# Kernel tuning notes

Measured on AMD Instinct MI355X. Metric: run time of the kernel, lower is better.

The kernel has to match this reference:

```python
import jax, jax.numpy as jnp
import numpy as np

B, L, D = 2, 2048, 1024
H = 16
HD = D // H  # 64


def _orthogonal_projection(key, d, m):
    g = jax.random.normal(key, (d, m), dtype=jnp.float32)
    q, r = jnp.linalg.qr(g)
    s = jnp.sign(jnp.diagonal(r))
    s = jnp.where(s == 0, 1.0, s)
    q = q * s[None, :]
    # preserve_variance=True
    return q * np.sqrt(d / m)


def setup_inputs() -> dict:
    key = jax.random.key(0)
    ks = jax.random.split(key, 8)
    x = jax.random.normal(ks[0], (B, L, D), dtype=jnp.float32)
    p = jax.random.normal(ks[1], (B, L, D), dtype=jnp.float32)
    s = 1.0 / np.sqrt(D)
    W_qkv = jax.random.uniform(ks[2], (3 * D, D), dtype=jnp.float32, minval=-s, maxval=s)
    b_qkv = jax.random.uniform(ks[3], (3 * D,), dtype=jnp.float32, minval=-s, maxval=s)
    W_out = jax.random.uniform(ks[4], (D, D), dtype=jnp.float32, minval=-s, maxval=s)
    b_out = jax.random.uniform(ks[5], (D,), dtype=jnp.float32, minval=-s, maxval=s)
    proj = _orthogonal_projection(ks[6], D, D // 2)
    return {"x": x, "p": p, "W_qkv": W_qkv, "b_qkv": b_qkv,
            "W_out": W_out, "b_out": b_out, "proj": proj}


def reference(x, p, W_qkv, b_qkv, W_out, b_out, proj):
    # QKV projection: (B,L,D) -> (B,L,3,H,HD)
    qkv = (jnp.einsum('bld,ed->ble', x, W_qkv) + b_qkv).reshape(B, L, 3, H, HD)
    q, k, v = qkv[:, :, 0], qkv[:, :, 1], qkv[:, :, 2]

    # Collaborative rotary phases from conditioning tokens: (B,L,H,HD/2)
    phases = (p @ proj).reshape(B, L, H, HD // 2)  # phase_scale = 1.0
    cos, sin = jnp.cos(phases), jnp.sin(phases)

    half = HD // 2
    # non-interleaved rotary: split head_dim into two halves
    def rot(t):
        t1, t2 = t[..., :half], t[..., half:]
        return jnp.concatenate([t1 * cos - t2 * sin, t1 * sin + t2 * cos], axis=-1)

    q, k = rot(q), rot(k)

    scale = HD ** -0.5
    scores = jnp.einsum('bqhd,bkhd->bhqk', q, k) * scale
    attn = jax.nn.softmax(scores, axis=-1)
    out = jnp.einsum('bhqk,bkhd->bqhd', attn, v).reshape(B, L, D)
    return jnp.einsum('bld,ed->ble', out, W_out) + b_out
```

## Files before the change

kernel.cpp:

```cpp
#include <hip/hip_runtime.h>
#include <hip/hip_bf16.h>
#include <math.h>

namespace {
constexpr int Bb = 2;
constexpr int Ll = 2048;
constexpr int Dd = 1024;
constexpr int Hh = 16;
constexpr int NT = Bb * Ll;
constexpr int D3 = 3 * Dd;
constexpr int PH = Dd / 2;
constexpr int LDK = 72;
}

typedef __attribute__((ext_vector_type(8))) short bf16x8;
typedef __attribute__((ext_vector_type(4))) short bf16x4;
typedef __attribute__((ext_vector_type(4))) float f32x4;

#if defined(__has_builtin)
#if __has_builtin(__builtin_amdgcn_mfma_f32_16x16x16bf16_1k)
#define HAVE_MFMA16 1
#endif
#endif

__device__ inline unsigned pack2bf(float a, float b) {
  __hip_bfloat162 t = __float22bfloat162_rn(float2{a, b});
  union { __hip_bfloat162 h; unsigned u; } cv; cv.h = t;
  return cv.u;
}

__device__ inline bf16x4 u2bf4(uint2 u) {
  union { uint2 u; bf16x4 v; } c; c.u = u; return c.v;
}

__device__ inline f32x4 pv_mfma(bf16x4 va, bf16x4 vb, f32x4 c) {
#ifdef HAVE_MFMA16
  return __builtin_amdgcn_mfma_f32_16x16x16bf16_1k(va, vb, c, 0, 0, 0);
#else
  const bf16x8 a8 = {va[0], va[1], va[2], va[3], 0, 0, 0, 0};
  const bf16x8 b8 = {vb[0], vb[1], vb[2], vb[3], 0, 0, 0, 0};
  return __builtin_amdgcn_mfma_f32_16x16x32_bf16(a8, b8, c, 0, 0, 0);
#endif
}

__device__ inline void async_cp16(const void* gsrc, void* ldst) {
  __builtin_amdgcn_global_load_lds(
      (const __attribute__((address_space(1))) unsigned int*)gsrc,
      (__attribute__((address_space(3))) unsigned int*)ldst, 16, 0, 0);
}

__global__ __launch_bounds__(256) void cast4_kernel(
    const float4* __restrict__ src, uint2* __restrict__ dst, int n4)
{
  const int i = blockIdx.x * 256 + threadIdx.x;
  if (i >= n4) return;
  const float4 f = src[i];
  dst[i] = make_uint2(pack2bf(f.x, f.y), pack2bf(f.z, f.w));
}

__global__ __launch_bounds__(256) void split_cast_kernel(
    const float4* __restrict__ src, uint2* __restrict__ hi, uint2* __restrict__ lo, int n4)
{
  const int i = blockIdx.x * 256 + threadIdx.x;
  if (i >= n4) return;
  const float4 f = src[i];
  float hf[4], lf[4];
  const float ff[4] = {f.x, f.y, f.z, f.w};
#pragma unroll
  for (int j = 0; j < 4; ++j) {
    const __hip_bfloat16 h = __float2bfloat16(ff[j]);
    hf[j] = __bfloat162float(h);
    lf[j] = ff[j] - hf[j];
  }
  hi[i] = make_uint2(pack2bf(hf[0], hf[1]), pack2bf(hf[2], hf[3]));
  lo[i] = make_uint2(pack2bf(lf[0], lf[1]), pack2bf(lf[2], lf[3]));
}

__global__ __launch_bounds__(256) void trans_split_kernel(
    const float* __restrict__ proj, short* __restrict__ th, short* __restrict__ tl)
{
  __shared__ float Ls[64][65];
  const int tid = threadIdx.x;
  const int d0 = blockIdx.x * 64, m0 = blockIdx.y * 64;
  const int r = tid >> 4, c4 = (tid & 15) * 4;
#pragma unroll
  for (int it = 0; it < 4; ++it) {
    const int row = it * 16 + r;
    const float4 v = *(const float4*)&proj[(size_t)(d0 + row) * PH + m0 + c4];
    Ls[row][c4] = v.x; Ls[row][c4+1] = v.y; Ls[row][c4+2] = v.z; Ls[row][c4+3] = v.w;
  }
  __syncthreads();
#pragma unroll
  for (int it = 0; it < 4; ++it) {
    const int row = it * 16 + r;
    float hf[4], lf[4];
#pragma unroll
    for (int j = 0; j < 4; ++j) {
      const float v = Ls[c4 + j][row];
      const __hip_bfloat16 h = __float2bfloat16(v);
      hf[j] = __bfloat162float(h);
      lf[j] = v - hf[j];
    }
    *(uint2*)&th[(size_t)(m0 + row) * Dd + d0 + c4] = make_uint2(pack2bf(hf[0], hf[1]), pack2bf(hf[2], hf[3]));
    *(uint2*)&tl[(size_t)(m0 + row) * Dd + d0 + c4] = make_uint2(pack2bf(lf[0], lf[1]), pack2bf(lf[2], lf[3]));
  }
}

__global__ __launch_bounds__(256) void gemm_nn_split(
    const short* __restrict__ Ah_g, const short* __restrict__ Al_g,
    const short* __restrict__ Wh_g, const short* __restrict__ Wl_g,
    float* __restrict__ C)
{
  __shared__ __align__(16) short Ah[64 * 32], Al[64 * 32], Wh[64 * 32], Wl[64 * 32];
  const int tid = threadIdx.x;
  const int w = tid >> 6, lane = tid & 63;
  const int l15 = lane & 15, quad = lane >> 4;
  const int wn = w >> 1, wm = w & 1;
  const int n0 = blockIdx.y * 64, m0 = blockIdx.x * 64;

  const int row = tid >> 2, cc = tid & 3;
  const int ksw = (cc ^ (row & 3)) * 8;
  const short* gAh = Ah_g + (size_t)(n0 + row) * Dd + ksw;
  const short* gAl = Al_g + (size_t)(n0 + row) * Dd + ksw;
  const short* gWh = Wh_g + (size_t)(m0 + row) * Dd + ksw;
  const short* gWl = Wl_g + (size_t)(m0 + row) * Dd + ksw;
  short* lAh = Ah + tid * 8;
  short* lAl = Al + tid * 8;
  short* lWh = Wh + tid * 8;
  short* lWl = Wl + tid * 8;

  f32x4 acc[2][2];
#pragma unroll
  for (int i = 0; i < 2; ++i)
#pragma unroll
    for (int j = 0; j < 2; ++j) acc[i][j] = f32x4{0.f, 0.f, 0.f, 0.f};

  const int swq = (quad ^ (l15 & 3)) * 8;

  for (int k0 = 0; k0 < Dd; k0 += 32) {
    __syncthreads();
    async_cp16(gAh + k0, lAh);
    async_cp16(gAl + k0, lAl);
    async_cp16(gWh + k0, lWh);
    async_cp16(gWl + k0, lWl);
    __syncthreads();

    bf16x8 ah[2], al[2], wh[2], wl[2];
#pragma unroll
    for (int i = 0; i < 2; ++i) {
      ah[i] = *(const bf16x8*)&Ah[(wn * 32 + i * 16 + l15) * 32 + swq];
      al[i] = *(const bf16x8*)&Al[(wn * 32 + i * 16 + l15) * 32 + swq];
    }
#pragma unroll
    for (int j = 0; j < 2; ++j) {
      wh[j] = *(const bf16x8*)&Wh[(wm * 32 + j * 16 + l15) * 32 + swq];
      wl[j] = *(const bf16x8*)&Wl[(wm * 32 + j * 16 + l15) * 32 + swq];
    }
#pragma unroll
    for (int i = 0; i < 2; ++i)
#pragma unroll
      for (int j = 0; j < 2; ++j) {
        acc[i][j] = __builtin_amdgcn_mfma_f32_16x16x32_bf16(ah[i], wh[j], acc[i][j], 0, 0, 0);
        acc[i][j] = __builtin_amdgcn_mfma_f32_16x16x32_bf16(ah[i], wl[j], acc[i][j], 0, 0, 0);
        acc[i][j] = __builtin_amdgcn_mfma_f32_16x16x32_bf16(al[i], wh[j], acc[i][j], 0, 0, 0);
      }
  }

#pragma unroll
  for (int i = 0; i < 2; ++i)
#pragma unroll
    for (int r = 0; r < 4; ++r) {
      float* crow = C + (size_t)(n0 + wn * 32 + i * 16 + quad * 4 + r) * PH + m0 + wm * 32 + l15;
#pragma unroll
      for (int j = 0; j < 2; ++j) crow[j * 16] = acc[i][j][r];
    }
}

__global__ __launch_bounds__(256) void gemm_bt_bf16(
    const __hip_bfloat16* __restrict__ A, const __hip_bfloat16* __restrict__ W,
    const float* __restrict__ bias, float* __restrict__ C, int K, int M)
{
  __shared__ __align__(16) short As[128 * 32];
  __shared__ __align__(16) short Ws[128 * 32];
  const int tid = threadIdx.x;
  const int w = tid >> 6, lane = tid & 63;
  const int l15 = lane & 15, quad = lane >> 4;
  const int wn = w >> 1, wm = w & 1;
  const int n0 = blockIdx.y * 128, m0 = blockIdx.x * 128;

  const int row = tid >> 2, cc = tid & 3;
  const int ksw = (cc ^ (row & 3)) * 8;
  const short* gA  = (const short*)A + (size_t)(n0 + row) * K + ksw;
  const short* gW  = (const short*)W + (size_t)(m0 + row) * K + ksw;
  short* lA  = As + tid * 8;
  short* lA2 = As + 2048 + tid * 8;
  short* lW  = Ws + tid * 8;
  short* lW2 = Ws + 2048 + tid * 8;

  f32x4 acc[4][4];
#pragma unroll
  for (int i = 0; i < 4; ++i)
#pragma unroll
    for (int j = 0; j < 4; ++j) acc[i][j] = f32x4{0.f, 0.f, 0.f, 0.f};

  const int swq = (quad ^ (l15 & 3)) * 8;

  for (int k0 = 0; k0 < K; k0 += 32) {
    __syncthreads();
    async_cp16(gA + k0, lA);
    async_cp16(gA + 64 * K + k0, lA2);
    async_cp16(gW + k0, lW);
    async_cp16(gW + 64 * K + k0, lW2);
    __syncthreads();

    bf16x8 af[4], bf[4];
#pragma unroll
    for (int i = 0; i < 4; ++i)
      af[i] = *(const bf16x8*)&As[(wn * 64 + i * 16 + l15) * 32 + swq];
#pragma unroll
    for (int j = 0; j < 4; ++j)
      bf[j] = *(const bf16x8*)&Ws[(wm * 64 + j * 16 + l15) * 32 + swq];
#pragma unroll
    for (int i = 0; i < 4; ++i)
#pragma unroll
      for (int j = 0; j < 4; ++j)
        acc[i][j] = __builtin_amdgcn_mfma_f32_16x16x32_bf16(af[i], bf[j], acc[i][j], 0, 0, 0);
  }

  float bv[4];
#pragma unroll
  for (int j = 0; j < 4; ++j) bv[j] = bias[m0 + wm * 64 + j * 16 + l15];
#pragma unroll
  for (int i = 0; i < 4; ++i)
#pragma unroll
    for (int r = 0; r < 4; ++r) {
      float* crow = C + (size_t)(n0 + wn * 64 + i * 16 + quad * 4 + r) * M + m0 + wm * 64 + l15;
#pragma unroll
      for (int j = 0; j < 4; ++j) crow[j * 16] = acc[i][j][r] + bv[j];
    }
}

__global__ __launch_bounds__(256) void rot_cast_kernel(
    const float* __restrict__ phases, const float* __restrict__ qkv,
    __hip_bfloat16* __restrict__ q_bf, __hip_bfloat16* __restrict__ k_bf)
{
  const int gid = blockIdx.x * 256 + threadIdx.x;
  const int i = gid & 31;
  const int h = (gid >> 5) & 15;
  const int n = gid >> 9;
  const float ph = phases[n * PH + h * 32 + i];
  float sn, cs;
  __sincosf(ph, &sn, &cs);
  const int base = n * D3 + h * 64 + i;
  const float q1 = qkv[base], q2 = qkv[base + 32];
  const float k1 = qkv[base + Dd], k2 = qkv[base + Dd + 32];
  const float SC = 0.18033688011112042f;
  const int ob = n * Dd + h * 64 + i;
  q_bf[ob]      = __float2bfloat16((q1 * cs - q2 * sn) * SC);
  q_bf[ob + 32] = __float2bfloat16((q1 * sn + q2 * cs) * SC);
  k_bf[ob]      = __float2bfloat16(k1 * cs - k2 * sn);
  k_bf[ob + 32] = __float2bfloat16(k1 * sn + k2 * cs);
}

__global__ __launch_bounds__(256) void vtrans_kernel(
    const float* __restrict__ qkv, __hip_bfloat16* __restrict__ vt_g)
{
  __shared__ __align__(16) short Vl[64 * LDK];
  const int tid = threadIdx.x;
  const int tt = blockIdx.x;
  const int bh = blockIdx.y;
  const int b = bh >> 4, h = bh & 15;

  {
    const int tok = tid >> 2, ds = tid & 3;
    const float* src = qkv + (size_t)(b * Ll + tt * 64 + tok) * D3 + 2 * Dd + h * 64 + ds * 16;
    unsigned* dstw = (unsigned*)&Vl[tok * LDK + ds * 16];
#pragma unroll
    for (int jj = 0; jj < 4; ++jj) {
      const float4 f = *(const float4*)(src + jj * 4);
      dstw[jj*2]   = pack2bf(f.x, f.y);
      dstw[jj*2+1] = pack2bf(f.z, f.w);
    }
  }
  __syncthreads();
  {
    const int d = tid >> 2, seg = tid & 3;
    unsigned ow[8];
#pragma unroll
    for (int j = 0; j < 8; ++j) {
      const unsigned short a = (unsigned short)Vl[(seg*16 + 2*j)     * LDK + d];
      const unsigned short c = (unsigned short)Vl[(seg*16 + 2*j + 1) * LDK + d];
      ow[j] = (unsigned)a | ((unsigned)c << 16);
    }
    unsigned* dst = (unsigned*)(vt_g + ((size_t)(bh * 64 + d)) * Ll + tt * 64 + seg * 16);
    *(uint4*)(dst)     = make_uint4(ow[0], ow[1], ow[2], ow[3]);
    *(uint4*)(dst + 4) = make_uint4(ow[4], ow[5], ow[6], ow[7]);
  }
}

__global__ __launch_bounds__(256) void attn_mfma(
    const __hip_bfloat16* __restrict__ q_bf,
    const __hip_bfloat16* __restrict__ k_bf,
    const __hip_bfloat16* __restrict__ vt_g,
    __hip_bfloat16* __restrict__ aout)
{
  __shared__ __align__(16) short Ks[64 * LDK];
  __shared__ __align__(16) short Vt[64 * LDK];

  const int tid = threadIdx.x;
  const int w = tid >> 6;
  const int lane = tid & 63;
  const int l15 = lane & 15;
  const int quad = lane >> 4;

  const int q0 = blockIdx.x * 128;
  const int bh = blockIdx.y;
  const int b = bh >> 4, h = bh & 15;

  bf16x8 qfrag[2][2];
#pragma unroll
  for (int qg = 0; qg < 2; ++qg)
#pragma unroll
    for (int kh = 0; kh < 2; ++kh) {
      const size_t qrow = (size_t)(b * Ll + q0 + w * 32 + qg * 16 + l15);
      qfrag[qg][kh] = *(const bf16x8*)(q_bf + qrow * Dd + h * 64 + kh * 32 + quad * 8);
    }

  f32x4 acc[4][2];
#pragma unroll
  for (int dt = 0; dt < 4; ++dt)
#pragma unroll
    for (int qg = 0; qg < 2; ++qg) acc[dt][qg] = f32x4{0.f, 0.f, 0.f, 0.f};
  float l_acc[2] = {0.f, 0.f};

  const int srow = tid >> 2, sseg = tid & 3;
  const __hip_bfloat16* kbase = k_bf + (size_t)(b * Ll + srow) * Dd + h * 64 + sseg * 16;
  const __hip_bfloat16* vbase = vt_g + ((size_t)(bh * 64 + srow)) * Ll + sseg * 16;

  for (int kt = 0; kt < Ll / 64; ++kt) {
    __syncthreads();
    {
      const uint4* kg = (const uint4*)(kbase + (size_t)kt * 64 * Dd);
      *(uint4*)&Ks[srow * LDK + sseg * 16]     = kg[0];
      *(uint4*)&Ks[srow * LDK + sseg * 16 + 8] = kg[1];
      const uint4* vg = (const uint4*)(vbase + kt * 64);
      *(uint4*)&Vt[srow * LDK + sseg * 16]     = vg[0];
      *(uint4*)&Vt[srow * LDK + sseg * 16 + 8] = vg[1];
    }
    __syncthreads();

    f32x4 s[4][2];
#pragma unroll
    for (int n = 0; n < 4; ++n)
#pragma unroll
      for (int qg = 0; qg < 2; ++qg) s[n][qg] = f32x4{0.f, 0.f, 0.f, 0.f};
#pragma unroll
    for (int n = 0; n < 4; ++n)
#pragma unroll
      for (int kh = 0; kh < 2; ++kh) {
        const bf16x8 af = *(const bf16x8*)&Ks[(n * 16 + l15) * LDK + kh * 32 + quad * 8];
        s[n][0] = __builtin_amdgcn_mfma_f32_16x16x32_bf16(af, qfrag[0][kh], s[n][0], 0, 0, 0);
        s[n][1] = __builtin_amdgcn_mfma_f32_16x16x32_bf16(af, qfrag[1][kh], s[n][1], 0, 0, 0);
      }

    uint2 bq[4][2];
#pragma unroll
    for (int qg = 0; qg < 2; ++qg)
#pragma unroll
      for (int n = 0; n < 4; ++n) {
        const float p0 = __builtin_amdgcn_exp2f(s[n][qg][0]);
        const float p1 = __builtin_amdgcn_exp2f(s[n][qg][1]);
        const float p2 = __builtin_amdgcn_exp2f(s[n][qg][2]);
        const float p3 = __builtin_amdgcn_exp2f(s[n][qg][3]);
        l_acc[qg] += (p0 + p1) + (p2 + p3);
        bq[n][qg] = make_uint2(pack2bf(p0, p1), pack2bf(p2, p3));
      }

#pragma unroll
    for (int n = 0; n < 4; ++n) {
      const bf16x4 pb0 = u2bf4(bq[n][0]);
      const bf16x4 pb1 = u2bf4(bq[n][1]);
#pragma unroll
      for (int dt = 0; dt < 4; ++dt) {
        const bf16x4 va = *(const bf16x4*)&Vt[(dt * 16 + l15) * LDK + n * 16 + quad * 4];
        acc[dt][0] = pv_mfma(va, pb0, acc[dt][0]);
        acc[dt][1] = pv_mfma(va, pb1, acc[dt][1]);
      }
    }
  }

#pragma unroll
  for (int qg = 0; qg < 2; ++qg) {
    float l = l_acc[qg];
    l += __shfl_xor(l, 16);
    l += __shfl_xor(l, 32);
    const float linv = 1.f / l;
    const size_t q = (size_t)(b * Ll + q0 + w * 32 + qg * 16 + l15);
#pragma unroll
    for (int dt = 0; dt < 4; ++dt) {
      const uint2 o = make_uint2(
          pack2bf(acc[dt][qg][0] * linv, acc[dt][qg][1] * linv),
          pack2bf(acc[dt][qg][2] * linv, acc[dt][qg][3] * linv));
      *(uint2*)&aout[q * Dd + h * 64 + dt * 16 + quad * 4] = o;
    }
  }
}

extern "C" void kernel_launch(void* const* d_in, const int* in_sizes, int n_in,
                              void* d_out, int out_size, void* d_ws, size_t ws_size,
                              hipStream_t stream) {
  const float* x     = (const float*)d_in[0];
  const float* p     = (const float*)d_in[1];
  const float* W_qkv = (const float*)d_in[2];
  const float* b_qkv = (const float*)d_in[3];
  const float* W_out = (const float*)d_in[4];
  const float* b_out = (const float*)d_in[5];
  const float* proj  = (const float*)d_in[6];
  float* out = (float*)d_out;

  char* wsb = (char*)d_ws;
  float*          phases   = (float*)(wsb);
  __hip_bfloat16* vt_g     = (__hip_bfloat16*)(wsb);
  short*          p_hi     = (short*)(wsb + (8u << 20));
  short*          p_lo     = (short*)(wsb + (16u << 20));
  short*          projt_hi = (short*)(wsb + (24u << 20));
  short*          projt_lo = (short*)(wsb + (25u << 20));
  float*          qkv      = (float*)(wsb + (8u << 20));
  __hip_bfloat16* aout_bf  = (__hip_bfloat16*)(wsb + (8u << 20));
  __hip_bfloat16* wout_bf  = (__hip_bfloat16*)(wsb + (16u << 20));
  __hip_bfloat16* x_bf     = (__hip_bfloat16*)(wsb + (56u << 20));
  __hip_bfloat16* q_bf     = (__hip_bfloat16*)(wsb + (56u << 20));
  __hip_bfloat16* wqkv_bf  = (__hip_bfloat16*)(wsb + (64u << 20));
  __hip_bfloat16* k_bf     = (__hip_bfloat16*)(wsb + (64u << 20));

  split_cast_kernel<<<4096, 256, 0, stream>>>((const float4*)p, (uint2*)p_hi, (uint2*)p_lo, 1048576);
  trans_split_kernel<<<dim3(Dd / 64, PH / 64), 256, 0, stream>>>(proj, projt_hi, projt_lo);
  gemm_nn_split<<<dim3(PH / 64, NT / 64), 256, 0, stream>>>(p_hi, p_lo, projt_hi, projt_lo, phases);
  cast4_kernel<<<4096, 256, 0, stream>>>((const float4*)x, (uint2*)x_bf, 1048576);
  cast4_kernel<<<3072, 256, 0, stream>>>((const float4*)W_qkv, (uint2*)wqkv_bf, 786432);
  gemm_bt_bf16<<<dim3(D3 / 128, NT / 128), 256, 0, stream>>>(x_bf, wqkv_bf, b_qkv, qkv, Dd, D3);
  rot_cast_kernel<<<dim3((NT * Hh * 32) / 256), 256, 0, stream>>>(phases, qkv, q_bf, k_bf);
  vtrans_kernel<<<dim3(Ll / 64, Bb * Hh), 256, 0, stream>>>(qkv, vt_g);
  cast4_kernel<<<1024, 256, 0, stream>>>((const float4*)W_out, (uint2*)wout_bf, 262144);
  attn_mfma<<<dim3(Ll / 128, Bb * Hh), 256, 0, stream>>>(q_bf, k_bf, vt_g, aout_bf);
  gemm_bt_bf16<<<dim3(Dd / 128, NT / 128), 256, 0, stream>>>(aout_bf, wout_bf, b_out, out, Dd, Dd);
}
```

Before: 284.6 us.

## Fuse rotary, scaling and V transpose into QKV GEMM epilogue; merge casts

The QKV GEMM epilogue now applies bias, the rotary rotation with sincos of the phases, and the Q scale, and writes bf16 Q/K directly. It also writes V transposed in bf16, which removes the fp32 qkv buffer and the separate rot_cast and vtrans kernels. The three fp32-to-bf16 casts are merged into one launch. In attention, the row-sum is accumulated from the bf16-truncated probabilities via a perm instruction instead of rounding, so the sum is consistent with the values fed to the PV product. The trade-offs are a heavier GEMM epilogue with scattered 2-byte stores and a different bf16 rounding mode (truncation).

```diff
diff --git a/kernel.cpp b/kernel.cpp
--- a/kernel.cpp
+++ b/kernel.cpp
@@ -49,13 +49,18 @@
       (__attribute__((address_space(3))) unsigned int*)ldst, 16, 0, 0);
 }
 
-__global__ __launch_bounds__(256) void cast4_kernel(
-    const float4* __restrict__ src, uint2* __restrict__ dst, int n4)
-{
-  const int i = blockIdx.x * 256 + threadIdx.x;
-  if (i >= n4) return;
-  const float4 f = src[i];
-  dst[i] = make_uint2(pack2bf(f.x, f.y), pack2bf(f.z, f.w));
+__global__ __launch_bounds__(256) void cast3_kernel(
+    const float4* __restrict__ x, const float4* __restrict__ wq,
+    const float4* __restrict__ wo,
+    uint2* __restrict__ xd, uint2* __restrict__ wqd, uint2* __restrict__ wod)
+{
+  int i = blockIdx.x * 256 + threadIdx.x;
+  const float4* s; uint2* d;
+  if (i < 1048576) { s = x; d = xd; }
+  else if (i < 1048576 + 786432) { i -= 1048576; s = wq; d = wqd; }
+  else { i -= 1048576 + 786432; s = wo; d = wod; }
+  const float4 f = s[i];
+  d[i] = make_uint2(pack2bf(f.x, f.y), pack2bf(f.z, f.w));
 }
 
 __global__ __launch_bounds__(256) void split_cast_kernel(
@@ -176,6 +181,104 @@
     }
 }
 
+__global__ __launch_bounds__(256) void gemm_qkv_fused(
+    const __hip_bfloat16* __restrict__ A, const __hip_bfloat16* __restrict__ W,
+    const float* __restrict__ bias, const float* __restrict__ phases,
+    __hip_bfloat16* __restrict__ q_bf, __hip_bfloat16* __restrict__ k_bf,
+    __hip_bfloat16* __restrict__ vt_g)
+{
+  __shared__ __align__(16) short As[128 * 32];
+  __shared__ __align__(16) short Ws[128 * 32];
+  const int tid = threadIdx.x;
+  const int w = tid >> 6, lane = tid & 63;
+  const int l15 = lane & 15, quad = lane >> 4;
+  const int wn = w >> 1, wm = w & 1;
+  const int n0 = blockIdx.y * 128, m0 = blockIdx.x * 128;
+
+  const int row = tid >> 2, cc = tid & 3;
+  const int ksw = (cc ^ (row & 3)) * 8;
+  const short* gA  = (const short*)A + (size_t)(n0 + row) * Dd + ksw;
+  const short* gW  = (const short*)W + (size_t)(m0 + row) * Dd + ksw;
+  short* lA  = As + tid * 8;
+  short* lA2 = As + 2048 + tid * 8;
+  short* lW  = Ws + tid * 8;
+  short* lW2 = Ws + 2048 + tid * 8;
+
+  f32x4 acc[4][4];
+#pragma unroll
+  for (int i = 0; i < 4; ++i)
+#pragma unroll
+    for (int j = 0; j < 4; ++j) acc[i][j] = f32x4{0.f, 0.f, 0.f, 0.f};
+
+  const int swq = (quad ^ (l15 & 3)) * 8;
+
+  for (int k0 = 0; k0 < Dd; k0 += 32) {
+    __syncthreads();
+    async_cp16(gA + k0, lA);
+    async_cp16(gA + 64 * Dd + k0, lA2);
+    async_cp16(gW + k0, lW);
+    async_cp16(gW + 64 * Dd + k0, lW2);
+    __syncthreads();
+
+    bf16x8 af[4], bf[4];
+#pragma unroll
+    for (int i = 0; i < 4; ++i)
+      af[i] = *(const bf16x8*)&As[(wn * 64 + i * 16 + l15) * 32 + swq];
+#pragma unroll
+    for (int j = 0; j < 4; ++j)
+      bf[j] = *(const bf16x8*)&Ws[(wm * 64 + j * 16 + l15) * 32 + swq];
+#pragma unroll
+    for (int i = 0; i < 4; ++i)
+#pragma unroll
+      for (int j = 0; j < 4; ++j)
+        acc[i][j] = __builtin_amdgcn_mfma_f32_16x16x32_bf16(af[i], bf[j], acc[i][j], 0, 0, 0);
+  }
+
+  float bv[4];
+#pragma unroll
+  for (int j = 0; j < 4; ++j) bv[j] = bias[m0 + wm * 64 + j * 16 + l15];
+
+  const int region = m0 >> 10;
+  const int mloc = (m0 & 1023) + wm * 64;
+  const int h = mloc >> 6;
+
+  if (region < 2) {
+    __hip_bfloat16* dst = region == 0 ? q_bf : k_bf;
+    const float SC = region == 0 ? 0.18033688011112042f : 1.0f;
+#pragma unroll
+    for (int i = 0; i < 4; ++i)
+#pragma unroll
+      for (int r = 0; r < 4; ++r) {
+        const int n = n0 + wn * 64 + i * 16 + quad * 4 + r;
+        const float* phrow = phases + (size_t)n * PH + h * 32;
+        __hip_bfloat16* drow = dst + (size_t)n * Dd + h * 64;
+#pragma unroll
+        for (int pz = 0; pz < 2; ++pz) {
+          const float ph = phrow[pz * 16 + l15];
+          float sn, cs;
+          __sincosf(ph, &sn, &cs);
+          const float a1 = acc[i][pz][r] + bv[pz];
+          const float a2 = acc[i][pz + 2][r] + bv[pz + 2];
+          drow[pz * 16 + l15]      = __float2bfloat16((a1 * cs - a2 * sn) * SC);
+          drow[pz * 16 + 32 + l15] = __float2bfloat16((a1 * sn + a2 * cs) * SC);
+        }
+      }
+  } else {
+    const int bh = (n0 >> 11) * 16 + h;
+    const int tokb = (n0 & 2047) + wn * 64;
+#pragma unroll
+    for (int i = 0; i < 4; ++i)
+#pragma unroll
+      for (int j = 0; j < 4; ++j) {
+        const uint2 o = make_uint2(
+            pack2bf(acc[i][j][0] + bv[j], acc[i][j][1] + bv[j]),
+            pack2bf(acc[i][j][2] + bv[j], acc[i][j][3] + bv[j]));
+        const int d = j * 16 + l15;
+        *(uint2*)&vt_g[(size_t)(bh * 64 + d) * Ll + tokb + i * 16 + quad * 4] = o;
+      }
+  }
+}
+
 __global__ __launch_bounds__(256) void gemm_bt_bf16(
     const __hip_bfloat16* __restrict__ A, const __hip_bfloat16* __restrict__ W,
     const float* __restrict__ bias, float* __restrict__ C, int K, int M)
@@ -240,64 +343,6 @@
     }
 }
 
-__global__ __launch_bounds__(256) void rot_cast_kernel(
-    const float* __restrict__ phases, const float* __restrict__ qkv,
-    __hip_bfloat16* __restrict__ q_bf, __hip_bfloat16* __restrict__ k_bf)
-{
-  const int gid = blockIdx.x * 256 + threadIdx.x;
-  const int i = gid & 31;
-  const int h = (gid >> 5) & 15;
-  const int n = gid >> 9;
-  const float ph = phases[n * PH + h * 32 + i];
-  float sn, cs;
-  __sincosf(ph, &sn, &cs);
-  const int base = n * D3 + h * 64 + i;
-  const float q1 = qkv[base], q2 = qkv[base + 32];
-  const float k1 = qkv[base + Dd], k2 = qkv[base + Dd + 32];
-  const float SC = 0.18033688011112042f;
-  const int ob = n * Dd + h * 64 + i;
-  q_bf[ob]      = __float2bfloat16((q1 * cs - q2 * sn) * SC);
-  q_bf[ob + 32] = __float2bfloat16((q1 * sn + q2 * cs) * SC);
-  k_bf[ob]      = __float2bfloat16(k1 * cs - k2 * sn);
-  k_bf[ob + 32] = __float2bfloat16(k1 * sn + k2 * cs);
-}
-
-__global__ __launch_bounds__(256) void vtrans_kernel(
-    const float* __restrict__ qkv, __hip_bfloat16* __restrict__ vt_g)
-{
-  __shared__ __align__(16) short Vl[64 * LDK];
-  const int tid = threadIdx.x;
-  const int tt = blockIdx.x;
-  const int bh = blockIdx.y;
-  const int b = bh >> 4, h = bh & 15;
-
-  {
-    const int tok = tid >> 2, ds = tid & 3;
-    const float* src = qkv + (size_t)(b * Ll + tt * 64 + tok) * D3 + 2 * Dd + h * 64 + ds * 16;
-    unsigned* dstw = (unsigned*)&Vl[tok * LDK + ds * 16];
-#pragma unroll
-    for (int jj = 0; jj < 4; ++jj) {
-      const float4 f = *(const float4*)(src + jj * 4);
-      dstw[jj*2]   = pack2bf(f.x, f.y);
-      dstw[jj*2+1] = pack2bf(f.z, f.w);
-    }
-  }
-  __syncthreads();
-  {
-    const int d = tid >> 2, seg = tid & 3;
-    unsigned ow[8];
-#pragma unroll
-    for (int j = 0; j < 8; ++j) {
-      const unsigned short a = (unsigned short)Vl[(seg*16 + 2*j)     * LDK + d];
-      const unsigned short c = (unsigned short)Vl[(seg*16 + 2*j + 1) * LDK + d];
-      ow[j] = (unsigned)a | ((unsigned)c << 16);
-    }
-    unsigned* dst = (unsigned*)(vt_g + ((size_t)(bh * 64 + d)) * Ll + tt * 64 + seg * 16);
-    *(uint4*)(dst)     = make_uint4(ow[0], ow[1], ow[2], ow[3]);
-    *(uint4*)(dst + 4) = make_uint4(ow[4], ow[5], ow[6], ow[7]);
-  }
-}
-
 __global__ __launch_bounds__(256) void attn_mfma(
     const __hip_bfloat16* __restrict__ q_bf,
     const __hip_bfloat16* __restrict__ k_bf,
@@ -368,12 +413,17 @@
     for (int qg = 0; qg < 2; ++qg)
 #pragma unroll
       for (int n = 0; n < 4; ++n) {
-        const float p0 = __builtin_amdgcn_exp2f(s[n][qg][0]);
-        const float p1 = __builtin_amdgcn_exp2f(s[n][qg][1]);
-        const float p2 = __builtin_amdgcn_exp2f(s[n][qg][2]);
-        const float p3 = __builtin_amdgcn_exp2f(s[n][qg][3]);
-        l_acc[qg] += (p0 + p1) + (p2 + p3);
-        bq[n][qg] = make_uint2(pack2bf(p0, p1), pack2bf(p2, p3));
+        union { float f; unsigned u; } p0, p1, p2, p3, t0, t1, t2, t3;
+        p0.f = __builtin_amdgcn_exp2f(s[n][qg][0]);
+        p1.f = __builtin_amdgcn_exp2f(s[n][qg][1]);
+        p2.f = __builtin_amdgcn_exp2f(s[n][qg][2]);
+        p3.f = __builtin_amdgcn_exp2f(s[n][qg][3]);
+        const unsigned lo = __builtin_amdgcn_perm(p1.u, p0.u, 0x07060302u);
+        const unsigned hi = __builtin_amdgcn_perm(p3.u, p2.u, 0x07060302u);
+        bq[n][qg] = make_uint2(lo, hi);
+        t0.u = lo << 16; t1.u = lo & 0xffff0000u;
+        t2.u = hi << 16; t3.u = hi & 0xffff0000u;
+        l_acc[qg] += (t0.f + t1.f) + (t2.f + t3.f);
       }
 
 #pragma unroll
@@ -420,28 +470,25 @@
 
   char* wsb = (char*)d_ws;
   float*          phases   = (float*)(wsb);
-  __hip_bfloat16* vt_g     = (__hip_bfloat16*)(wsb);
   short*          p_hi     = (short*)(wsb + (8u << 20));
+  __hip_bfloat16* aout_bf  = (__hip_bfloat16*)(wsb + (8u << 20));
   short*          p_lo     = (short*)(wsb + (16u << 20));
+  __hip_bfloat16* vt_g     = (__hip_bfloat16*)(wsb + (16u << 20));
   short*          projt_hi = (short*)(wsb + (24u << 20));
   short*          projt_lo = (short*)(wsb + (25u << 20));
-  float*          qkv      = (float*)(wsb + (8u << 20));
-  __hip_bfloat16* aout_bf  = (__hip_bfloat16*)(wsb + (8u << 20));
-  __hip_bfloat16* wout_bf  = (__hip_bfloat16*)(wsb + (16u << 20));
-  __hip_bfloat16* x_bf     = (__hip_bfloat16*)(wsb + (56u << 20));
-  __hip_bfloat16* q_bf     = (__hip_bfloat16*)(wsb + (56u << 20));
-  __hip_bfloat16* wqkv_bf  = (__hip_bfloat16*)(wsb + (64u << 20));
-  __hip_bfloat16* k_bf     = (__hip_bfloat16*)(wsb + (64u << 20));
+  __hip_bfloat16* q_bf     = (__hip_bfloat16*)(wsb + (26u << 20));
+  __hip_bfloat16* k_bf     = (__hip_bfloat16*)(wsb + (34u << 20));
+  __hip_bfloat16* x_bf     = (__hip_bfloat16*)(wsb + (42u << 20));
+  __hip_bfloat16* wqkv_bf  = (__hip_bfloat16*)(wsb + (50u << 20));
+  __hip_bfloat16* wout_bf  = (__hip_bfloat16*)(wsb + (56u << 20));
 
   split_cast_kernel<<<4096, 256, 0, stream>>>((const float4*)p, (uint2*)p_hi, (uint2*)p_lo, 1048576);
   trans_split_kernel<<<dim3(Dd / 64, PH / 64), 256, 0, stream>>>(proj, projt_hi, projt_lo);
+  cast3_kernel<<<8192, 256, 0, stream>>>((const float4*)x, (const float4*)W_qkv, (const float4*)W_out,
+                                         (uint2*)x_bf, (uint2*)wqkv_bf, (uint2*)wout_bf);
   gemm_nn_split<<<dim3(PH / 64, NT / 64), 256, 0, stream>>>(p_hi, p_lo, projt_hi, projt_lo, phases);
-  cast4_kernel<<<4096, 256, 0, stream>>>((const float4*)x, (uint2*)x_bf, 1048576);
-  cast4_kernel<<<3072, 256, 0, stream>>>((const float4*)W_qkv, (uint2*)wqkv_bf, 786432);
-  gemm_bt_bf16<<<dim3(D3 / 128, NT / 128), 256, 0, stream>>>(x_bf, wqkv_bf, b_qkv, qkv, Dd, D3);
-  rot_cast_kernel<<<dim3((NT * Hh * 32) / 256), 256, 0, stream>>>(phases, qkv, q_bf, k_bf);
-  vtrans_kernel<<<dim3(Ll / 64, Bb * Hh), 256, 0, stream>>>(qkv, vt_g);
-  cast4_kernel<<<1024, 256, 0, stream>>>((const float4*)W_out, (uint2*)wout_bf, 262144);
+  gemm_qkv_fused<<<dim3(D3 / 128, NT / 128), 256, 0, stream>>>(x_bf, wqkv_bf, b_qkv, phases,
+                                                               q_bf, k_bf, vt_g);
   attn_mfma<<<dim3(Ll / 128, Bb * Hh), 256, 0, stream>>>(q_bf, k_bf, vt_g, aout_bf);
   gemm_bt_bf16<<<dim3(Dd / 128, NT / 128), 256, 0, stream>>>(aout_bf, wout_bf, b_out, out, Dd, Dd);
 }
```

Measured after the change: 275.1 us. -3.3%, faster.
